# Performance work log

Measured on AMD Instinct MI355X. Metric: run time of the kernel, lower is better.

Reference implementation:

```python
import jax, jax.numpy as jnp
import numpy as np

N = 100000   # nodes
E = 600000   # edges
H = 128      # hidden_dim
G = 1000     # graphs in batch
BN_EPS = 1e-5


def setup_inputs() -> dict:
    key = jax.random.key(0)
    ks = jax.random.split(key, 24)
    inp = {}
    inp['x'] = jax.random.normal(ks[0], (N, 3), dtype=jnp.float32)
    inp['edge_index'] = jax.random.randint(ks[1], (2, E), 0, N, dtype=jnp.int64)
    inp['batch'] = jnp.sort(jax.random.randint(ks[2], (N,), 0, G, dtype=jnp.int64))
    # conv 0 (in=3)
    inp['W1_0'] = jax.random.normal(ks[3], (3, H), dtype=jnp.float32) * 0.3
    inp['b1_0'] = jax.random.normal(ks[4], (H,), dtype=jnp.float32) * 0.02
    inp['g_0'] = jax.random.uniform(ks[5], (H,), dtype=jnp.float32) + 0.5
    inp['be_0'] = jax.random.normal(ks[6], (H,), dtype=jnp.float32) * 0.02
    inp['m_0'] = jax.random.normal(ks[7], (H,), dtype=jnp.float32) * 0.02
    inp['v_0'] = jax.random.uniform(ks[8], (H,), dtype=jnp.float32) + 0.5
    inp['W2_0'] = jax.random.normal(ks[9], (H, H), dtype=jnp.float32) * 0.05
    inp['b2_0'] = jax.random.normal(ks[10], (H,), dtype=jnp.float32) * 0.02
    # convs 1..4 (in=H), stacked on leading axis
    inp['W1s'] = jax.random.normal(ks[11], (4, H, H), dtype=jnp.float32) * 0.05
    inp['b1s'] = jax.random.normal(ks[12], (4, H), dtype=jnp.float32) * 0.02
    inp['gs'] = jax.random.uniform(ks[13], (4, H), dtype=jnp.float32) + 0.5
    inp['bes'] = jax.random.normal(ks[14], (4, H), dtype=jnp.float32) * 0.02
    inp['ms'] = jax.random.normal(ks[15], (4, H), dtype=jnp.float32) * 0.02
    inp['vs'] = jax.random.uniform(ks[16], (4, H), dtype=jnp.float32) + 0.5
    inp['W2s'] = jax.random.normal(ks[17], (4, H, H), dtype=jnp.float32) * 0.05
    inp['b2s'] = jax.random.normal(ks[18], (4, H), dtype=jnp.float32) * 0.02
    inp['Wc'] = jax.random.normal(ks[19], (H, 1), dtype=jnp.float32) * 0.05
    inp['bc'] = jax.random.normal(ks[20], (1,), dtype=jnp.float32) * 0.02
    return inp


def _gin_conv(x, src, dst, W1, b1, g, be, m, v, W2, b2):
    # GINConv with eps=0: mlp(x + sum_{j in N(i)} x_j)
    agg = jax.ops.segment_sum(x[src], dst, num_segments=N)  # [N, d]
    h = x + agg
    h = h @ W1 + b1
    h = g * (h - m) * jax.lax.rsqrt(v + BN_EPS) + be  # BatchNorm (eval)
    h = jax.nn.relu(h)
    h = h @ W2 + b2
    return jax.nn.relu(h)  # outer F.relu in GIN.forward; dropout is identity (eval)


def reference(x, edge_index, batch, W1_0, b1_0, g_0, be_0, m_0, v_0, W2_0, b2_0,
              W1s, b1s, gs, bes, ms, vs, W2s, b2s, Wc, bc):
    src, dst = edge_index[0], edge_index[1]
    h = _gin_conv(x, src, dst, W1_0, b1_0, g_0, be_0, m_0, v_0, W2_0, b2_0)
    for l in range(4):  # fixed small layer loop
        h = _gin_conv(h, src, dst, W1s[l], b1s[l], gs[l], bes[l], ms[l], vs[l], W2s[l], b2s[l])
    pooled = jax.ops.segment_sum(h, batch, num_segments=G)  # [G, H] global_add_pool
    return (pooled @ Wc + bc).reshape(-1)  # [G]
```

## Files before the change

kernel.cpp:

```cpp
#include <hip/hip_runtime.h>

#define NN 100000
#define EE 600000
#define HH 128
#define GG 1000
#define NPAD 100096
#define NBLK2 1564

typedef __attribute__((ext_vector_type(8))) short bf16x8;
typedef __attribute__((ext_vector_type(4))) float f32x4;
typedef _Float16 f16;

__device__ inline short f2bf(float x){
    unsigned u = __float_as_uint(x);
    unsigned r = (u + 0x7FFFu + ((u >> 16) & 1u)) >> 16;
    return (short)r;
}
__device__ inline float bf2f(short h){
    unsigned u = ((unsigned)(unsigned short)h) << 16;
    return __uint_as_float(u);
}
__device__ inline float2 cvt2(unsigned u){
    f16 lo = ((const f16*)&u)[0];
    f16 hi = ((const f16*)&u)[1];
    return make_float2((float)lo, (float)hi);
}

#define GLD(dst, voff, sbase) \
    asm volatile("global_load_dword %0, %1, %2" \
                 : "=v"(dst) : "v"(voff), "s"(sbase) : "memory")

#define WAITV(N) do { \
    asm volatile("s_waitcnt vmcnt(" #N ")" ::: "memory"); \
    __builtin_amdgcn_sched_barrier(0); \
} while (0)

__global__ void k_hist(const int* __restrict__ dst, int* __restrict__ cnt){
    int e = blockIdx.x*256 + threadIdx.x;
    if (e < EE) atomicAdd(&cnt[dst[e]], 1);
}

__global__ void k_scan1(const int* __restrict__ cnt, int* __restrict__ excl,
                        int* __restrict__ bsums, int n){
    __shared__ int wsum[4];
    int t = threadIdx.x;
    int idx = blockIdx.x*1024 + t*4;
    int c[4];
#pragma unroll
    for (int i = 0; i < 4; i++) c[i] = (idx+i < n) ? cnt[idx+i] : 0;
    int s = c[0]+c[1]+c[2]+c[3];
    int lane = t & 63, w = t >> 6;
    int x = s;
#pragma unroll
    for (int off = 1; off < 64; off <<= 1){
        int y = __shfl_up(x, off);
        if (lane >= off) x += y;
    }
    if (lane == 63) wsum[w] = x;
    __syncthreads();
    int woff = 0;
    for (int i = 0; i < w; i++) woff += wsum[i];
    int run = woff + x - s;
#pragma unroll
    for (int i = 0; i < 4; i++){
        if (idx+i < n) excl[idx+i] = run;
        run += c[i];
    }
    if (t == 255) bsums[blockIdx.x] = woff + x;
}

__global__ void k_scan2(int* __restrict__ bsums, int nb){
    __shared__ int ws2[2];
    int t = threadIdx.x;
    int v = (t < nb) ? bsums[t] : 0;
    int lane = t & 63, w = t >> 6;
    int x = v;
#pragma unroll
    for (int off = 1; off < 64; off <<= 1){
        int y = __shfl_up(x, off);
        if (lane >= off) x += y;
    }
    if (lane == 63) ws2[w] = x;
    __syncthreads();
    int off0 = (w == 1) ? ws2[0] : 0;
    if (t < nb) bsums[t] = off0 + x - v;
}

__global__ void k_scan3(int* __restrict__ rp, const int* __restrict__ bsums,
                        int* __restrict__ fill, int n){
    int i = blockIdx.x*256 + threadIdx.x;
    if (i < n){
        int r = rp[i] + bsums[i >> 10];
        rp[i] = r;
        fill[i] = r;
    }
    if (i == 0) rp[n] = EE;
}

__global__ void k_place(const int* __restrict__ src, const int* __restrict__ dst,
                        int* __restrict__ fill, int* __restrict__ spk){
    int e = blockIdx.x*256 + threadIdx.x;
    if (e < EE){
        int d = dst[e];
        int p = atomicAdd(&fill[d], 1);
        spk[p] = (src[e] << 4) | (d & 15);
    }
}

__global__ void k_init(const int* __restrict__ batch, int* __restrict__ fill,
                       int* __restrict__ rp_g,
                       const float* __restrict__ W2_0, const float* __restrict__ W1s,
                       const float* __restrict__ W2s, short* __restrict__ Wp){
    int tid = blockIdx.x*256 + threadIdx.x;
    if (tid < NN){
        fill[tid] = 0;
        int b = batch[tid];
        if (tid == 0){
            for (int g = 0; g <= b; g++) rp_g[g] = 0;
        } else {
            int p = batch[tid-1];
            for (int g = p+1; g <= b; g++) rp_g[g] = tid;
        }
        if (tid == NN-1){
            for (int g = b+1; g <= GG; g++) rp_g[g] = NN;
        }
    }
    if (tid < 9*16384){
        int m = tid >> 14;
        int r = tid & 16383;
        int j = r & 7, l = (r >> 3) & 63, ctkc = r >> 9;
        int ct = ctkc & 7, kc = ctkc >> 3;
        int k = kc*32 + ((l >> 4) << 3) + j;
        int n = (ct << 4) + (l & 15);
        const float* W = (m == 0) ? W2_0
                       : (m <= 4) ? (W1s + (size_t)(m-1)*HH*HH)
                                  : (W2s + (size_t)(m-5)*HH*HH);
        float w = W[k*HH + n];
        short hi = f2bf(w);
        short lo = f2bf(w - bf2f(hi));
        short* base = Wp + (size_t)m*32768;
        base[r] = hi;
        base[16384 + r] = lo;
    }
}

__global__ void k_agg3(const float* __restrict__ x, const int* __restrict__ rp,
                       const int* __restrict__ spk, float* __restrict__ y){
    int i = blockIdx.x*256 + threadIdx.x;
    if (i >= NN) return;
    float a0 = x[3*i], a1 = x[3*i+1], a2 = x[3*i+2];
    int b = rp[i], e = rp[i+1];
    for (int k = b; k < e; k++){
        int s = spk[k] >> 4;
        a0 += x[3*s]; a1 += x[3*s+1]; a2 += x[3*s+2];
    }
    y[3*i] = a0; y[3*i+1] = a1; y[3*i+2] = a2;
}


__device__ inline void wave_gemm(const short* __restrict__ sAh,
                                 const short* __restrict__ sAl,
                                 const short* __restrict__ Wp,
                                 int n, int q, f32x4* acc){
    const short* Wh = Wp;
    const short* Wl = Wp + 16384;
    const int l = (q << 4) | n;
#pragma unroll
    for (int ct = 0; ct < 8; ct++) acc[ct] = (f32x4){0.f,0.f,0.f,0.f};
#pragma unroll
    for (int kc = 0; kc < 4; kc++){
        int c = (q << 4) | (n & 8) | ((n & 7) ^ ((q & 1) << 2) ^ kc);
        int pos = kc*512 + c*8;
        bf16x8 ah = *(const bf16x8*)&sAh[pos];
        bf16x8 al = *(const bf16x8*)&sAl[pos];
        const short* ph = Wh + (size_t)(kc*8)*512 + l*8;
        const short* pl = Wl + (size_t)(kc*8)*512 + l*8;
#pragma unroll
        for (int ct = 0; ct < 8; ct++){
            bf16x8 bh = *(const bf16x8*)(ph + ct*512);
            bf16x8 bl = *(const bf16x8*)(pl + ct*512);
            acc[ct] = __builtin_amdgcn_mfma_f32_16x16x32_bf16(ah, bh, acc[ct], 0, 0, 0);
            acc[ct] = __builtin_amdgcn_mfma_f32_16x16x32_bf16(al, bh, acc[ct], 0, 0, 0);
            acc[ct] = __builtin_amdgcn_mfma_f32_16x16x32_bf16(ah, bl, acc[ct], 0, 0, 0);
        }
    }
}

__global__ __launch_bounds__(256, 4)
void k_layer0(const float* __restrict__ y0, const short* __restrict__ Wp,
              const float* __restrict__ W1, const float* __restrict__ b1,
              const float* __restrict__ g, const float* __restrict__ be,
              const float* __restrict__ m, const float* __restrict__ v,
              const float* __restrict__ b2, f16* __restrict__ out){
    __shared__ __align__(16) char smem[32768];
    const int t = threadIdx.x;
    const int w = t >> 6, l = t & 63;
    short* sAh = (short*)(smem + w*8192);
    short* sAl = (short*)(smem + w*8192 + 4096);
    const int R0 = blockIdx.x*64 + w*16;

    {
        int hw = l >> 5, ln = l & 31;
        int c4 = ln << 2;
        int kc1 = ln >> 3, q1 = (ln >> 1) & 3, j1 = (ln & 1) << 2;
        float Wc[3][4], Ac[4], Bc[4];
#pragma unroll
        for (int i = 0; i < 4; i++){
            int c = c4 + i;
            float rs = rsqrtf(v[c] + 1e-5f);
            float sc = g[c]*rs;
            Ac[i] = sc;
            Bc[i] = sc*(b1[c] - m[c]) + be[c];
            Wc[0][i] = W1[c]; Wc[1][i] = W1[HH + c]; Wc[2][i] = W1[2*HH + c];
        }
        float ya[8], yb[8], yc[8];
#pragma unroll
        for (int it = 0; it < 8; it++){
            int node = R0 + hw + (it << 1);
            ya[it] = y0[3*node]; yb[it] = y0[3*node+1]; yc[it] = y0[3*node+2];
        }
#pragma unroll
        for (int it = 0; it < 8; it++){
            int mm = hw + (it << 1);
            float xs[4];
#pragma unroll
            for (int i = 0; i < 4; i++){
                float raw = ya[it]*Wc[0][i] + yb[it]*Wc[1][i] + yc[it]*Wc[2][i];
                xs[i] = fmaxf(fmaf(raw, Ac[i], Bc[i]), 0.f);
            }
            int c = (q1 << 4) | (mm & 8) | ((mm & 7) ^ ((q1 & 1) << 2) ^ kc1);
            int pos = kc1*512 + c*8 + j1;
            unsigned hp[2], lp[2];
#pragma unroll
            for (int i = 0; i < 2; i++){
                unsigned u0 = __float_as_uint(xs[2*i]);
                unsigned u1 = __float_as_uint(xs[2*i+1]);
                float r0 = xs[2*i]   - __uint_as_float(u0 & 0xFFFF0000u);
                float r1 = xs[2*i+1] - __uint_as_float(u1 & 0xFFFF0000u);
                hp[i] = (u0 >> 16) | (u1 & 0xFFFF0000u);
                lp[i] = (__float_as_uint(r0) >> 16) | (__float_as_uint(r1) & 0xFFFF0000u);
            }
            *(uint2*)&sAh[pos] = make_uint2(hp[0], hp[1]);
            *(uint2*)&sAl[pos] = make_uint2(lp[0], lp[1]);
        }
    }
    __asm__ volatile("" ::: "memory");

    const int n = l & 15, q = l >> 4;
    f32x4 acc[8];
    wave_gemm(sAh, sAl, Wp, n, q, acc);
#pragma unroll
    for (int ct = 0; ct < 8; ct++){
        int j = (ct << 4) + n;
        float shv = b2[j];
#pragma unroll
        for (int r = 0; r < 4; r++){
            int row = R0 + q*4 + r;
            out[(size_t)row*HH + j] = (f16)fmaxf(acc[ct][r] + shv, 0.f);
        }
    }
}

__device__ __forceinline__ int sidx(int r, int k){
    return r*128 + (k ^ ((r & 7) << 2));
}

__device__ __forceinline__ void wave_gemm_f32(const float* __restrict__ sF,
                                              const short* __restrict__ Wp,
                                              int l, f32x4* acc){
    const short* Wh = Wp;
    const short* Wl = Wp + 16384;
    const int rw = l & 15, q = l >> 4;
    const int v7 = (rw & 7) << 2;
    const int rbase = rw << 7;
#pragma unroll
    for (int ct = 0; ct < 8; ct++) acc[ct] = (f32x4){0.f,0.f,0.f,0.f};
#pragma unroll
    for (int kc = 0; kc < 4; kc++){
        int k0 = kc*32 + (q << 3);
        float4 fa = *(const float4*)&sF[rbase + ((k0    ) ^ v7)];
        float4 fb = *(const float4*)&sF[rbase + ((k0 + 4) ^ v7)];
        float xs[8] = {fa.x,fa.y,fa.z,fa.w,fb.x,fb.y,fb.z,fb.w};
        bf16x8 ah, al;
#pragma unroll
        for (int i = 0; i < 8; i++){
            unsigned u = __float_as_uint(xs[i]);
            ah[i] = (short)(u >> 16);
            float rv = xs[i] - __uint_as_float(u & 0xFFFF0000u);
            al[i] = (short)(__float_as_uint(rv) >> 16);
        }
        const short* ph = Wh + (size_t)(kc*8)*512 + l*8;
        const short* pl = Wl + (size_t)(kc*8)*512 + l*8;
#pragma unroll
        for (int ct = 0; ct < 8; ct++){
            bf16x8 bh = *(const bf16x8*)(ph + ct*512);
            bf16x8 bl = *(const bf16x8*)(pl + ct*512);
            acc[ct] = __builtin_amdgcn_mfma_f32_16x16x32_bf16(ah, bh, acc[ct], 0, 0, 0);
            acc[ct] = __builtin_amdgcn_mfma_f32_16x16x32_bf16(al, bh, acc[ct], 0, 0, 0);
            acc[ct] = __builtin_amdgcn_mfma_f32_16x16x32_bf16(ah, bl, acc[ct], 0, 0, 0);
        }
    }
}

#define PROC_EDGE(uval, sival) do { \
    int lr_ = (sival) & 15; \
    if (lr_ != cur){ \
        if (cur >= 0){ \
            int off_ = cur*128 + ((2*l) ^ ((cur & 7) << 2)); \
            *(float2*)&sF[off_] = make_float2(acc0, acc1); \
        } \
        cur = lr_; \
        int off_ = lr_*128 + ((2*l) ^ ((lr_ & 7) << 2)); \
        float2 sv_ = *(const float2*)&sF[off_]; \
        acc0 = sv_.x; acc1 = sv_.y; \
    } \
    float2 fv_ = cvt2(uval); \
    acc0 += fv_.x; acc1 += fv_.y; \
} while (0)

#define ISSUE_CHUNK(U, J) do { \
    _Pragma("unroll") \
    for (int j_ = 0; j_ < 32; j_++){ \
        int sj_ = __builtin_amdgcn_readlane((J), j_) >> 4; \
        GLD(U[j_], voff, A2 + (size_t)sj_*64); \
    } \
} while (0)

#define ISSUE_TAIL(U, J) do { \
    _Pragma("unroll") \
    for (int j_ = 0; j_ < 32; j_++){ \
        if (j_ < remT){ \
            int sj_ = __builtin_amdgcn_readlane((J), j_) >> 4; \
            GLD(U[j_], voff, A2 + (size_t)sj_*64); \
        } \
    } \
} while (0)

#define PROC_CHUNK(U, J) do { \
    _Pragma("unroll") \
    for (int j_ = 0; j_ < 32; j_++){ \
        int si_ = __builtin_amdgcn_readlane((J), j_); \
        PROC_EDGE(U[j_], si_); \
    } \
} while (0)

#define PROC_TAIL(U, J) do { \
    _Pragma("unroll") \
    for (int j_ = 0; j_ < 32; j_++){ \
        if (j_ < remT){ \
            int si_ = __builtin_amdgcn_readlane((J), j_); \
            PROC_EDGE(U[j_], si_); \
        } \
    } \
} while (0)

__global__ __launch_bounds__(256, 3)
void k_layer(const f16* __restrict__ A, const int* __restrict__ rp,
             const int* __restrict__ spk,
             const short* __restrict__ Wp1, const short* __restrict__ Wp2,
             const float* __restrict__ b1, const float* __restrict__ g,
             const float* __restrict__ be, const float* __restrict__ m,
             const float* __restrict__ v, const float* __restrict__ b2,
             f16* __restrict__ out){
    __shared__ __align__(16) float smemf[8192];
    const int t = threadIdx.x;
    const int w = t >> 6, l = t & 63;
    float* sF = smemf + w*2048;
    const int r0w = blockIdx.x*64 + w*16;
    const unsigned* A2 = (const unsigned*)A;

    {
        int half = l >> 5, lm = l & 31;
        int k0 = lm << 2;
#pragma unroll
        for (int i = 0; i < 8; i++){
            int r = (i << 1) + half;
            uint2 u = *(const uint2*)&A2[(size_t)(r0w + r)*64 + (lm << 1)];
            float2 f0 = cvt2(u.x), f1 = cvt2(u.y);
            int base = r*128 + (k0 ^ ((r & 7) << 2));
            *(float4*)&sF[base] = make_float4(f0.x, f0.y, f1.x, f1.y);
        }
    }

    {
        int rlo = r0w < NN ? r0w : NN;
        int rhi = (r0w + 16) < NN ? (r0w + 16) : NN;
        int elo = __builtin_amdgcn_readfirstlane(rp[rlo]);
        int ehi = __builtin_amdgcn_readfirstlane(rp[rhi]);
        int nE  = ehi - elo;
        int nfull = nE >> 5;
        int remT  = nE & 31;
        int voff = l << 2;
        int vio  = (l & 31) << 2;
        float acc0 = 0.f, acc1 = 0.f;
        int cur = -1;
        unsigned U0[32], U1[32];
        int J0, J1, J2, J3;
        const int* sp = spk + elo;

        if (nfull == 0){
            if (remT > 0){
                GLD(J0, vio, sp);
                WAITV(0);
                ISSUE_TAIL(U0, J0);
                WAITV(0);
                PROC_TAIL(U0, J0);
            }
        } else {
            GLD(J0, vio, sp);
            GLD(J1, vio, sp + 32);
            WAITV(0);
            ISSUE_CHUNK(U0, J0);
            GLD(J2, vio, sp + 64);
            GLD(J3, vio, sp + 96);

            int c = 0;
            while (c + 4 < nfull){
                ISSUE_CHUNK(U1, J1);
                WAITV(34);
                PROC_CHUNK(U0, J0);
                WAITV(33);
                GLD(J0, vio, sp + c*32 + 128);
                ISSUE_CHUNK(U0, J2);
                WAITV(33);
                PROC_CHUNK(U1, J1);
                GLD(J1, vio, sp + c*32 + 160);
                ISSUE_CHUNK(U1, J3);
                WAITV(33);
                PROC_CHUNK(U0, J2);
                ISSUE_CHUNK(U0, J0);
                GLD(J2, vio, sp + c*32 + 192);
                WAITV(33);
                PROC_CHUNK(U1, J3);
                GLD(J3, vio, sp + c*32 + 224);
                c += 4;
            }

            int rem = nfull - c;
            if (rem == 1){
                ISSUE_TAIL(U1, J1);
                WAITV(0);
                PROC_CHUNK(U0, J0);
                PROC_TAIL(U1, J1);
            } else if (rem == 2){
                ISSUE_CHUNK(U1, J1);
                WAITV(34);
                PROC_CHUNK(U0, J0);
                WAITV(33);
                ISSUE_TAIL(U0, J2);
                WAITV(0);
                PROC_CHUNK(U1, J1);
                PROC_TAIL(U0, J2);
            } else if (rem == 3){
                ISSUE_CHUNK(U1, J1);
                WAITV(34);
                PROC_CHUNK(U0, J0);
                WAITV(33);
                ISSUE_CHUNK(U0, J2);
                WAITV(32);
                PROC_CHUNK(U1, J1);
                ISSUE_TAIL(U1, J3);
                WAITV(0);
                PROC_CHUNK(U0, J2);
                PROC_TAIL(U1, J3);
            } else {
                ISSUE_CHUNK(U1, J1);
                WAITV(34);
                PROC_CHUNK(U0, J0);
                WAITV(33);
                GLD(J0, vio, sp + c*32 + 128);
                ISSUE_CHUNK(U0, J2);
                WAITV(33);
                PROC_CHUNK(U1, J1);
                ISSUE_CHUNK(U1, J3);
                WAITV(32);
                PROC_CHUNK(U0, J2);
                ISSUE_TAIL(U0, J0);
                WAITV(0);
                PROC_CHUNK(U1, J3);
                PROC_TAIL(U0, J0);
            }
        }
        if (cur >= 0){
            int off = cur*128 + ((2*l) ^ ((cur & 7) << 2));
            *(float2*)&sF[off] = make_float2(acc0, acc1);
        }
        WAITV(0);
    }
    __asm__ volatile("" ::: "memory");

    const int n = l & 15, q = l >> 4;

    f32x4 acc[8];
    wave_gemm_f32(sF, Wp1, l, acc);
    __asm__ volatile("" ::: "memory");
#pragma unroll
    for (int ct = 0; ct < 8; ct++){
        int j = (ct << 4) + n;
        float rr = rsqrtf(v[j] + 1e-5f);
        float scv = g[j]*rr;
        float shv = be[j] + scv*(b1[j] - m[j]);
#pragma unroll
        for (int r = 0; r < 4; r++){
            int row = (q << 2) + r;
            float vv = fmaxf(fmaf(acc[ct][r], scv, shv), 0.f);
            sF[sidx(row, j)] = vv;
        }
    }
    __asm__ volatile("" ::: "memory");

    wave_gemm_f32(sF, Wp2, l, acc);
#pragma unroll
    for (int ct = 0; ct < 8; ct++){
        int j = (ct << 4) + n;
        float shv = b2[j];
#pragma unroll
        for (int r = 0; r < 4; r++){
            int row = r0w + (q << 2) + r;
            out[(size_t)row*HH + j] = (f16)fmaxf(acc[ct][r] + shv, 0.f);
        }
    }
}

__global__ void k_pool2(const f16* __restrict__ h, const float* __restrict__ Wc,
                        const float* __restrict__ bc, const int* __restrict__ rp_g,
                        float* __restrict__ out){
    __shared__ float ws[4];
    int g = blockIdx.x, t = threadIdx.x;
    const unsigned* h2 = (const unsigned*)h;
    long beg = (long)rp_g[g]*64, end = (long)rp_g[g+1]*64;
    float s = 0.f;
    for (long i = beg + t; i < end; i += 256){
        unsigned u = h2[i];
        int p = (int)(i & 63);
        float2 fv = cvt2(u);
        s += fv.x*Wc[2*p] + fv.y*Wc[2*p+1];
    }
    int lane = t & 63, w = t >> 6;
#pragma unroll
    for (int off = 32; off > 0; off >>= 1) s += __shfl_down(s, off);
    if (lane == 0) ws[w] = s;
    __syncthreads();
    if (t == 0) out[g] = bc[0] + ws[0] + ws[1] + ws[2] + ws[3];
}

extern "C" void kernel_launch(void* const* d_in, const int* in_sizes, int n_in,
                              void* d_out, int out_size, void* d_ws, size_t ws_size,
                              hipStream_t stream){
    const float* x     = (const float*)d_in[0];
    const int*   ei    = (const int*)d_in[1];
    const int*   batch = (const int*)d_in[2];
    const float* W1_0  = (const float*)d_in[3];
    const float* b1_0  = (const float*)d_in[4];
    const float* g_0   = (const float*)d_in[5];
    const float* be_0  = (const float*)d_in[6];
    const float* m_0   = (const float*)d_in[7];
    const float* v_0   = (const float*)d_in[8];
    const float* W2_0  = (const float*)d_in[9];
    const float* b2_0  = (const float*)d_in[10];
    const float* W1s   = (const float*)d_in[11];
    const float* b1s   = (const float*)d_in[12];
    const float* gs    = (const float*)d_in[13];
    const float* bes   = (const float*)d_in[14];
    const float* ms    = (const float*)d_in[15];
    const float* vs    = (const float*)d_in[16];
    const float* W2s   = (const float*)d_in[17];
    const float* b2s   = (const float*)d_in[18];
    const float* Wc    = (const float*)d_in[19];
    const float* bc    = (const float*)d_in[20];

    f16* H0 = (f16*)d_ws;
    f16* H1 = H0 + (size_t)NPAD*HH;
    int* rp    = (int*)(H1 + (size_t)NPAD*HH);
    int* fill  = rp + (NN + 1);
    int* spk   = fill + NN;
    int* bsums = spk + EE + 128;
    int* rp_g  = bsums + 128;
    size_t off = (size_t)((char*)(rp_g + (GG + 1)) - (char*)d_ws);
    off = (off + 15) & ~(size_t)15;
    short* Wp = (short*)((char*)d_ws + off);
    float* Y  = (float*)H1;

    const int* src = ei;
    const int* dst = ei + EE;

    k_init<<<(9*16384+255)/256, 256, 0, stream>>>(batch, fill, rp_g,
                                                  W2_0, W1s, W2s, Wp);

    k_hist<<<(EE+255)/256, 256, 0, stream>>>(dst, fill);
    k_scan1<<<98, 256, 0, stream>>>(fill, rp, bsums, NN);
    k_scan2<<<1, 128, 0, stream>>>(bsums, 98);
    k_scan3<<<(NN+255)/256, 256, 0, stream>>>(rp, bsums, fill, NN);
    k_place<<<(EE+255)/256, 256, 0, stream>>>(src, dst, fill, spk);

    k_agg3<<<(NN+255)/256, 256, 0, stream>>>(x, rp, spk, Y);
    k_layer0<<<NBLK2, 256, 0, stream>>>(Y, Wp, W1_0, b1_0, g_0, be_0, m_0, v_0,
                                        b2_0, H0);

    f16* cur = H0; f16* oth = H1;
    for (int l = 0; l < 4; l++){
        k_layer<<<NBLK2, 256, 0, stream>>>(cur, rp, spk,
                                           Wp + (size_t)(1+l)*32768,
                                           Wp + (size_t)(5+l)*32768,
                                           b1s + l*HH, gs + l*HH, bes + l*HH,
                                           ms + l*HH, vs + l*HH, b2s + l*HH,
                                           oth);
        f16* tmp = cur; cur = oth; oth = tmp;
    }

    k_pool2<<<GG, 256, 0, stream>>>(cur, Wc, bc, rp_g, (float*)d_out);
}
```

Before: 489.4 us.

## Replace inline-asm gather pipeline with compiler loads and halve layer block size

Swaps the hand-scheduled inline-asm global loads and explicit vmcnt waits in the edge-gather loop for plain C++ loads in a simpler double-buffered loop, leaving the compiler to schedule and wait. The layer kernel also shrinks from 256 to 128 threads per block (2 waves, 32 rows) and doubles the grid, halving shared memory per block so more blocks can be resident. The risk is that the compiler inserts conservative waits, losing the memory-level parallelism the manual schedule kept in flight. Index prefetch reads up to 64 entries past the current chunk, so it may read past the end of the index array for the last rows.

```diff
diff --git a/kernel.cpp b/kernel.cpp
--- a/kernel.cpp
+++ b/kernel.cpp
@@ -6,6 +6,7 @@
 #define GG 1000
 #define NPAD 100096
 #define NBLK2 1564
+#define NBLKL 3128
 
 typedef __attribute__((ext_vector_type(8))) short bf16x8;
 typedef __attribute__((ext_vector_type(4))) float f32x4;
@@ -25,15 +26,6 @@
     f16 hi = ((const f16*)&u)[1];
     return make_float2((float)lo, (float)hi);
 }
-
-#define GLD(dst, voff, sbase) \
-    asm volatile("global_load_dword %0, %1, %2" \
-                 : "=v"(dst) : "v"(voff), "s"(sbase) : "memory")
-
-#define WAITV(N) do { \
-    asm volatile("s_waitcnt vmcnt(" #N ")" ::: "memory"); \
-    __builtin_amdgcn_sched_barrier(0); \
-} while (0)
 
 __global__ void k_hist(const int* __restrict__ dst, int* __restrict__ cnt){
     int e = blockIdx.x*256 + threadIdx.x;
@@ -318,25 +310,25 @@
     acc0 += fv_.x; acc1 += fv_.y; \
 } while (0)
 
-#define ISSUE_CHUNK(U, J) do { \
+#define ISSUE_FULL(U, J) do { \
     _Pragma("unroll") \
     for (int j_ = 0; j_ < 32; j_++){ \
         int sj_ = __builtin_amdgcn_readlane((J), j_) >> 4; \
-        GLD(U[j_], voff, A2 + (size_t)sj_*64); \
+        U[j_] = A2[(size_t)sj_*64 + l]; \
     } \
 } while (0)
 
-#define ISSUE_TAIL(U, J) do { \
+#define ISSUE_PART(U, J) do { \
     _Pragma("unroll") \
     for (int j_ = 0; j_ < 32; j_++){ \
         if (j_ < remT){ \
             int sj_ = __builtin_amdgcn_readlane((J), j_) >> 4; \
-            GLD(U[j_], voff, A2 + (size_t)sj_*64); \
+            U[j_] = A2[(size_t)sj_*64 + l]; \
         } \
     } \
 } while (0)
 
-#define PROC_CHUNK(U, J) do { \
+#define PROC_FULL(U, J) do { \
     _Pragma("unroll") \
     for (int j_ = 0; j_ < 32; j_++){ \
         int si_ = __builtin_amdgcn_readlane((J), j_); \
@@ -344,7 +336,7 @@
     } \
 } while (0)
 
-#define PROC_TAIL(U, J) do { \
+#define PROC_PART(U, J) do { \
     _Pragma("unroll") \
     for (int j_ = 0; j_ < 32; j_++){ \
         if (j_ < remT){ \
@@ -354,7 +346,7 @@
     } \
 } while (0)
 
-__global__ __launch_bounds__(256, 3)
+__global__ __launch_bounds__(128, 4)
 void k_layer(const f16* __restrict__ A, const int* __restrict__ rp,
              const int* __restrict__ spk,
              const short* __restrict__ Wp1, const short* __restrict__ Wp2,
@@ -362,11 +354,11 @@
              const float* __restrict__ be, const float* __restrict__ m,
              const float* __restrict__ v, const float* __restrict__ b2,
              f16* __restrict__ out){
-    __shared__ __align__(16) float smemf[8192];
+    __shared__ __align__(16) float smemf[4096];
     const int t = threadIdx.x;
     const int w = t >> 6, l = t & 63;
     float* sF = smemf + w*2048;
-    const int r0w = blockIdx.x*64 + w*16;
+    const int r0w = blockIdx.x*32 + w*16;
     const unsigned* A2 = (const unsigned*)A;
 
     {
@@ -390,102 +382,47 @@
         int nE  = ehi - elo;
         int nfull = nE >> 5;
         int remT  = nE & 31;
-        int voff = l << 2;
-        int vio  = (l & 31) << 2;
+        int lm = l & 31;
         float acc0 = 0.f, acc1 = 0.f;
         int cur = -1;
-        unsigned U0[32], U1[32];
-        int J0, J1, J2, J3;
-        const int* sp = spk + elo;
-
-        if (nfull == 0){
-            if (remT > 0){
-                GLD(J0, vio, sp);
-                WAITV(0);
-                ISSUE_TAIL(U0, J0);
-                WAITV(0);
-                PROC_TAIL(U0, J0);
+        unsigned uA[32], uB[32];
+
+        int idxA = spk[elo + lm];
+        int idxB = spk[elo + 32 + lm];
+        int idxC = spk[elo + 64 + lm];
+
+        if (nfull > 0){
+            ISSUE_FULL(uA, idxA);
+        } else if (remT > 0){
+            ISSUE_PART(uA, idxA);
+        }
+
+        int c = 0;
+        while (c + 2 <= nfull){
+            ISSUE_FULL(uB, idxB);
+            int idxD = spk[elo + (c+3)*32 + lm];
+            int idxE = spk[elo + (c+4)*32 + lm];
+            PROC_FULL(uA, idxA);
+            if (c + 2 < nfull){
+                ISSUE_FULL(uA, idxC);
+            } else if (remT > 0){
+                ISSUE_PART(uA, idxC);
             }
+            PROC_FULL(uB, idxB);
+            idxA = idxC; idxB = idxD; idxC = idxE;
+            c += 2;
+        }
+        if (nfull - c == 1){
+            if (remT > 0) ISSUE_PART(uB, idxB);
+            PROC_FULL(uA, idxA);
+            if (remT > 0) PROC_PART(uB, idxB);
         } else {
-            GLD(J0, vio, sp);
-            GLD(J1, vio, sp + 32);
-            WAITV(0);
-            ISSUE_CHUNK(U0, J0);
-            GLD(J2, vio, sp + 64);
-            GLD(J3, vio, sp + 96);
-
-            int c = 0;
-            while (c + 4 < nfull){
-                ISSUE_CHUNK(U1, J1);
-                WAITV(34);
-                PROC_CHUNK(U0, J0);
-                WAITV(33);
-                GLD(J0, vio, sp + c*32 + 128);
-                ISSUE_CHUNK(U0, J2);
-                WAITV(33);
-                PROC_CHUNK(U1, J1);
-                GLD(J1, vio, sp + c*32 + 160);
-                ISSUE_CHUNK(U1, J3);
-                WAITV(33);
-                PROC_CHUNK(U0, J2);
-                ISSUE_CHUNK(U0, J0);
-                GLD(J2, vio, sp + c*32 + 192);
-                WAITV(33);
-                PROC_CHUNK(U1, J3);
-                GLD(J3, vio, sp + c*32 + 224);
-                c += 4;
-            }
-
-            int rem = nfull - c;
-            if (rem == 1){
-                ISSUE_TAIL(U1, J1);
-                WAITV(0);
-                PROC_CHUNK(U0, J0);
-                PROC_TAIL(U1, J1);
-            } else if (rem == 2){
-                ISSUE_CHUNK(U1, J1);
-                WAITV(34);
-                PROC_CHUNK(U0, J0);
-                WAITV(33);
-                ISSUE_TAIL(U0, J2);
-                WAITV(0);
-                PROC_CHUNK(U1, J1);
-                PROC_TAIL(U0, J2);
-            } else if (rem == 3){
-                ISSUE_CHUNK(U1, J1);
-                WAITV(34);
-                PROC_CHUNK(U0, J0);
-                WAITV(33);
-                ISSUE_CHUNK(U0, J2);
-                WAITV(32);
-                PROC_CHUNK(U1, J1);
-                ISSUE_TAIL(U1, J3);
-                WAITV(0);
-                PROC_CHUNK(U0, J2);
-                PROC_TAIL(U1, J3);
-            } else {
-                ISSUE_CHUNK(U1, J1);
-                WAITV(34);
-                PROC_CHUNK(U0, J0);
-                WAITV(33);
-                GLD(J0, vio, sp + c*32 + 128);
-                ISSUE_CHUNK(U0, J2);
-                WAITV(33);
-                PROC_CHUNK(U1, J1);
-                ISSUE_CHUNK(U1, J3);
-                WAITV(32);
-                PROC_CHUNK(U0, J2);
-                ISSUE_TAIL(U0, J0);
-                WAITV(0);
-                PROC_CHUNK(U1, J3);
-                PROC_TAIL(U0, J0);
-            }
+            if (remT > 0) PROC_PART(uA, idxA);
         }
         if (cur >= 0){
             int off = cur*128 + ((2*l) ^ ((cur & 7) << 2));
             *(float2*)&sF[off] = make_float2(acc0, acc1);
         }
-        WAITV(0);
     }
     __asm__ volatile("" ::: "memory");
 
@@ -599,7 +536,7 @@
 
     f16* cur = H0; f16* oth = H1;
     for (int l = 0; l < 4; l++){
-        k_layer<<<NBLK2, 256, 0, stream>>>(cur, rp, spk,
+        k_layer<<<NBLKL, 128, 0, stream>>>(cur, rp, spk,
                                            Wp + (size_t)(1+l)*32768,
                                            Wp + (size_t)(5+l)*32768,
                                            b1s + l*HH, gs + l*HH, bes + l*HH,
```

Result: faster. 433.9 us (-11.3%).
